# Optimization experiments

Hardware: AMD Instinct MI355X
Metric: run time of the kernel (lower is better)

The kernel has to match this reference:

```python
import jax, jax.numpy as jnp
import numpy as np
from jax import lax

N, EMB, AED, H, KCL = 4096, 768, 512, 8, 32
HD = AED // H
TEMP, THR, EPS, MAX_IT = 0.5, 1e-4, 1e-6, 100


def setup_inputs() -> dict:
    key = jax.random.key(0)
    ks = jax.random.split(key, 9)
    s = 0.02
    return {
        "embeddings": jax.random.normal(ks[0], (N, EMB), jnp.float32),
        "qw": jax.random.normal(ks[1], (EMB, AED), jnp.float32) * s,
        "kw": jax.random.normal(ks[2], (EMB, AED), jnp.float32) * s,
        "vw": jax.random.normal(ks[3], (EMB, AED), jnp.float32) * s,
        "in_proj_w": jax.random.normal(ks[4], (3 * AED, AED), jnp.float32) * s,
        "in_proj_b": jnp.zeros((3 * AED,), jnp.float32),
        "out_w": jax.random.normal(ks[5], (AED, AED), jnp.float32) * s,
        "out_b": jnp.zeros((AED,), jnp.float32),
        "init_idx": jax.random.randint(ks[6], (KCL,), 0, N, dtype=jnp.int32),
    }


def _mha(q, k, v, Wi, bi, Wo, bo):
    # torch nn.MultiheadAttention, batch_first, batch==1, no mask
    Wq, Wk, Wv = jnp.split(Wi, 3, axis=0)
    bq, bk, bv = jnp.split(bi, 3)
    n = q.shape[0]
    qh = (q @ Wq.T + bq).reshape(n, H, HD).transpose(1, 0, 2)  # [H,N,hd]
    kh = (k @ Wk.T + bk).reshape(n, H, HD).transpose(1, 0, 2)
    vh = (v @ Wv.T + bv).reshape(n, H, HD).transpose(1, 0, 2)
    scores = jnp.einsum("hqd,hkd->hqk", qh, kh) / jnp.sqrt(jnp.float32(HD))
    attn = jax.nn.softmax(scores, axis=-1)            # [H,N,N]
    o = jnp.einsum("hqk,hkd->hqd", attn, vh)          # [H,N,hd]
    o = o.transpose(1, 0, 2).reshape(n, AED)
    return o @ Wo.T + bo


def _cdist(X, C):
    # euclidean distance [N,K]
    d2 = (jnp.sum(X * X, 1)[:, None] + jnp.sum(C * C, 1)[None, :]
          - 2.0 * (X @ C.T))
    return jnp.sqrt(jnp.maximum(d2, 0.0))


def _dkm_step(X, C):
    a = jax.nn.softmax(-_cdist(X, C) / TEMP, axis=1)  # [N,K]
    a_sum = jnp.sum(a, axis=0) + EPS                  # [K]
    C_new = (a.T @ X) / a_sum[:, None]                # [K,E]
    return a, C_new


def _dkm(X, C_init):
    a, C_new = _dkm_step(X, C_init)
    diff = jnp.sum(jnp.abs(C_new - C_init))
    def body(carry, _):
        C, a, C_new, diff = carry
        cont = diff > THR
        C2 = jnp.where(cont, C_new, C)
        a2, C_new2 = _dkm_step(X, C2)
        a2 = jnp.where(cont, a2, a)
        C_new2 = jnp.where(cont, C_new2, C_new)
        diff2 = jnp.where(cont, jnp.sum(jnp.abs(C_new2 - C2)), diff)
        return (C2, a2, C_new2, diff2), None
    (C, a, _, _), _ = lax.scan(body, (C_init, a, C_new, diff), None, length=MAX_IT)
    return C, a


def reference(embeddings, qw, kw, vw, in_proj_w, in_proj_b, out_w, out_b, init_idx):
    q = embeddings @ qw
    k = embeddings @ kw
    v = embeddings @ vw
    tr = _mha(q, k, v, in_proj_w, in_proj_b, out_w, out_b)  # [N,AED]
    init_c = lax.stop_gradient(tr[init_idx])                # detached init
    C, a = _dkm(tr, init_c)
    return C, a
```

## Files before the change

### kernel.cpp

```cpp
#include <hip/hip_runtime.h>
#include <hip/hip_bf16.h>


typedef __hip_bfloat16 bf16;
typedef __attribute__((ext_vector_type(8))) short s16x8;
typedef __attribute__((ext_vector_type(4))) float f32x4;

__device__ __forceinline__ void  stv(float* p, float v) { *p = v; }
__device__ __forceinline__ void  stv(bf16*  p, float v) { *p = __float2bfloat16(v); }

__device__ __forceinline__ float gload(const float* p)
{
    return __hip_atomic_load(p, __ATOMIC_RELAXED, __HIP_MEMORY_SCOPE_AGENT);
}
__device__ __forceinline__ void gstore(float* p, float v)
{
    __hip_atomic_store(p, v, __ATOMIC_RELAXED, __HIP_MEMORY_SCOPE_AGENT);
}
__device__ __forceinline__ void gstore2(float2* p, float2 v)
{
    unsigned long long u; __builtin_memcpy(&u, &v, 8);
    __hip_atomic_store((unsigned long long*)p, u, __ATOMIC_RELAXED, __HIP_MEMORY_SCOPE_AGENT);
}

__device__ __forceinline__ unsigned bf16word(float v)
{
    bf16 b = __float2bfloat16(v);
    unsigned short u;
    __builtin_memcpy(&u, &b, 2);
    return ((unsigned)u) << 16;
}

__device__ __forceinline__ void stage8(const float* g, bf16* d)
{
    const float4 a = *(const float4*)g;
    const float4 b = *(const float4*)(g + 4);
    union { uint4 u; bf16 h[8]; } r;
    r.h[0] = __float2bfloat16(a.x); r.h[1] = __float2bfloat16(a.y);
    r.h[2] = __float2bfloat16(a.z); r.h[3] = __float2bfloat16(a.w);
    r.h[4] = __float2bfloat16(b.x); r.h[5] = __float2bfloat16(b.y);
    r.h[6] = __float2bfloat16(b.z); r.h[7] = __float2bfloat16(b.w);
    *(uint4*)d = r.u;
}
__device__ __forceinline__ void stage8(const bf16* g, bf16* d)
{
    *(uint4*)d = *(const uint4*)g;
}
__device__ __forceinline__ void load8f(const float* g, float* v)
{
    const float4 a = *(const float4*)g; const float4 b = *(const float4*)(g + 4);
    v[0]=a.x; v[1]=a.y; v[2]=a.z; v[3]=a.w; v[4]=b.x; v[5]=b.y; v[6]=b.z; v[7]=b.w;
}
__device__ __forceinline__ void load8f(const bf16* g, float* v)
{
    union { uint4 u; bf16 h[8]; } r; r.u = *(const uint4*)g;
#pragma unroll
    for (int j = 0; j < 8; j++) v[j] = __bfloat162float(r.h[j]);
}

struct P3 { const void* a[3]; const void* b[3]; const float* bi[3]; void* c[3]; };

template<typename TA, typename TB, typename TC, bool BT, bool BIAS>
__global__ __launch_bounds__(256) void mgemm(P3 p, int M, int N, int K)
{
    __shared__ __align__(16) bf16 As[64][40];
    __shared__ __align__(16) bf16 Bs[64][40];
    const int z = blockIdx.z;
    const TA* A = (const TA*)p.a[z];
    const TB* B = (const TB*)p.b[z];
    const float* bias = p.bi[z];
    TC* C = (TC*)p.c[z];
    const int m0 = blockIdx.x * 64, n0 = blockIdx.y * 64;
    const int t = threadIdx.x;
    const int w = t >> 6, lane = t & 63, quad = lane >> 4, l15 = lane & 15;
    f32x4 acc[4];
#pragma unroll
    for (int i = 0; i < 4; i++) acc[i] = (f32x4){0.f, 0.f, 0.f, 0.f};
    for (int k0 = 0; k0 < K; k0 += 32) {
        {
            int r = t >> 2, c = (t & 3) * 8;
            stage8(&A[(size_t)(m0 + r) * K + k0 + c], &As[r][c]);
        }
        if constexpr (BT) {
            int r = t >> 2, c = (t & 3) * 8;
            stage8(&B[(size_t)(n0 + r) * K + k0 + c], &Bs[r][c]);
        } else {
            int k = t >> 3, n8 = (t & 7) * 8;
            float v[8];
            load8f(&B[(size_t)(k0 + k) * N + n0 + n8], v);
#pragma unroll
            for (int j = 0; j < 8; j++) Bs[n8 + j][k] = __float2bfloat16(v[j]);
        }
        __syncthreads();
        s16x8 af = *(const s16x8*)&As[w * 16 + l15][quad * 8];
#pragma unroll
        for (int nt = 0; nt < 4; nt++) {
            s16x8 bfv = *(const s16x8*)&Bs[nt * 16 + l15][quad * 8];
            acc[nt] = __builtin_amdgcn_mfma_f32_16x16x32_bf16(af, bfv, acc[nt], 0, 0, 0);
        }
        __syncthreads();
    }
#pragma unroll
    for (int nt = 0; nt < 4; nt++) {
        int col = n0 + nt * 16 + l15;
        float bv = 0.f;
        if constexpr (BIAS) bv = bias[col];
#pragma unroll
        for (int r = 0; r < 4; r++) {
            int row = m0 + w * 16 + quad * 4 + r;
            stv(&C[(size_t)row * N + col], acc[nt][r] + bv);
        }
    }
}

__global__ __launch_bounds__(256) void attn_mfma(
    const bf16* __restrict__ qh, const bf16* __restrict__ kh,
    const bf16* __restrict__ vh, bf16* __restrict__ oatt)
{
    __shared__ __align__(16) bf16  Qs[64][72];
    __shared__ __align__(16) bf16  Ks[64][72];
    __shared__ __align__(16) bf16  Vt[64][72];
    __shared__ __align__(16) float Ss[64][68];
    __shared__ __align__(16) bf16  Ps[64][72];
    __shared__ float mrow[64], lrow[64], arow[64];
    const int bid = blockIdx.x;
    const int h = bid & 7, q0 = (bid >> 3) * 64;
    const int t = threadIdx.x;
    const int w = t >> 6, lane = t & 63, quad = lane >> 4, l15 = lane & 15;

#pragma unroll
    for (int i = 0; i < 2; i++) {
        int idx = t + i * 256;
        int r = idx >> 3, c = (idx & 7) * 8;
        *(uint4*)&Qs[r][c] = *(const uint4*)&qh[(size_t)(q0 + r) * 512 + h * 64 + c];
    }
    if (t < 64) { mrow[t] = -1e30f; lrow[t] = 0.f; }
    f32x4 accO[4];
#pragma unroll
    for (int i = 0; i < 4; i++) accO[i] = (f32x4){0.f, 0.f, 0.f, 0.f};

    const int sidx0 = t, sidx1 = t + 256;
    const int sr0 = sidx0 >> 3, sc0 = (sidx0 & 7) * 8;
    const int sr1 = sidx1 >> 3, sc1v = (sidx1 & 7) * 8;
    uint4 kreg0 = *(const uint4*)&kh[(size_t)sr0 * 512 + h * 64 + sc0];
    uint4 vreg0 = *(const uint4*)&vh[(size_t)sr0 * 512 + h * 64 + sc0];
    uint4 kreg1 = *(const uint4*)&kh[(size_t)sr1 * 512 + h * 64 + sc1v];
    uint4 vreg1 = *(const uint4*)&vh[(size_t)sr1 * 512 + h * 64 + sc1v];

    for (int kb = 0; kb < 4096; kb += 64) {
        __syncthreads();
        {
            *(uint4*)&Ks[sr0][sc0] = kreg0;
            union { uint4 u; bf16 b[8]; } vv; vv.u = vreg0;
            int rlo = sr0 & 7, rch = sr0 >> 3, rx = sidx0 & 7;
#pragma unroll
            for (int j = 0; j < 8; j++)
                Vt[sc0 + j][rlo | (((rch ^ rx) & 7) << 3)] = vv.b[j];
        }
        {
            *(uint4*)&Ks[sr1][sc1v] = kreg1;
            union { uint4 u; bf16 b[8]; } vv; vv.u = vreg1;
            int rlo = sr1 & 7, rch = sr1 >> 3, rx = sidx1 & 7;
#pragma unroll
            for (int j = 0; j < 8; j++)
                Vt[sc1v + j][rlo | (((rch ^ rx) & 7) << 3)] = vv.b[j];
        }
        __syncthreads();
        if (kb + 64 < 4096) {
            size_t base0 = (size_t)(kb + 64 + sr0) * 512 + h * 64;
            size_t base1 = (size_t)(kb + 64 + sr1) * 512 + h * 64;
            kreg0 = *(const uint4*)&kh[base0 + sc0];
            vreg0 = *(const uint4*)&vh[base0 + sc0];
            kreg1 = *(const uint4*)&kh[base1 + sc1v];
            vreg1 = *(const uint4*)&vh[base1 + sc1v];
        }
        f32x4 accS[4];
#pragma unroll
        for (int i = 0; i < 4; i++) accS[i] = (f32x4){0.f, 0.f, 0.f, 0.f};
        __builtin_amdgcn_s_setprio(1);
#pragma unroll
        for (int dc = 0; dc < 64; dc += 32) {
            s16x8 aq = *(const s16x8*)&Qs[w * 16 + l15][dc + quad * 8];
#pragma unroll
            for (int nt = 0; nt < 4; nt++) {
                s16x8 bk = *(const s16x8*)&Ks[nt * 16 + l15][dc + quad * 8];
                accS[nt] = __builtin_amdgcn_mfma_f32_16x16x32_bf16(aq, bk, accS[nt], 0, 0, 0);
            }
        }
        __builtin_amdgcn_s_setprio(0);
#pragma unroll
        for (int nt = 0; nt < 4; nt++)
#pragma unroll
            for (int r = 0; r < 4; r++)
                Ss[w * 16 + quad * 4 + r][nt * 16 + l15] = accS[nt][r] * 0.1803368801f;
        {
            const int srow = t >> 2, sseg = t & 3;
            float* sp = &Ss[srow][sseg * 16];
            float4 s0 = *(const float4*)(sp + 0);
            float4 s1 = *(const float4*)(sp + 4);
            float4 s2 = *(const float4*)(sp + 8);
            float4 s3 = *(const float4*)(sp + 12);
            float mold = mrow[srow];
            float m01 = fmaxf(fmaxf(s0.x, s0.y), fmaxf(s0.z, s0.w));
            float m23 = fmaxf(fmaxf(s1.x, s1.y), fmaxf(s1.z, s1.w));
            float m45 = fmaxf(fmaxf(s2.x, s2.y), fmaxf(s2.z, s2.w));
            float m67 = fmaxf(fmaxf(s3.x, s3.y), fmaxf(s3.z, s3.w));
            float mx = fmaxf(fmaxf(m01, m23), fmaxf(m45, m67));
            mx = fmaxf(mx, mold);
            mx = fmaxf(mx, __shfl_xor(mx, 1));
            mx = fmaxf(mx, __shfl_xor(mx, 2));
            s0.x = exp2f(s0.x - mx); s0.y = exp2f(s0.y - mx);
            s0.z = exp2f(s0.z - mx); s0.w = exp2f(s0.w - mx);
            s1.x = exp2f(s1.x - mx); s1.y = exp2f(s1.y - mx);
            s1.z = exp2f(s1.z - mx); s1.w = exp2f(s1.w - mx);
            s2.x = exp2f(s2.x - mx); s2.y = exp2f(s2.y - mx);
            s2.z = exp2f(s2.z - mx); s2.w = exp2f(s2.w - mx);
            s3.x = exp2f(s3.x - mx); s3.y = exp2f(s3.y - mx);
            s3.z = exp2f(s3.z - mx); s3.w = exp2f(s3.w - mx);
            union { uint4 u; bf16 h[8]; } pa, pb;
            pa.h[0] = __float2bfloat16(s0.x); pa.h[1] = __float2bfloat16(s0.y);
            pa.h[2] = __float2bfloat16(s0.z); pa.h[3] = __float2bfloat16(s0.w);
            pa.h[4] = __float2bfloat16(s1.x); pa.h[5] = __float2bfloat16(s1.y);
            pa.h[6] = __float2bfloat16(s1.z); pa.h[7] = __float2bfloat16(s1.w);
            pb.h[0] = __float2bfloat16(s2.x); pb.h[1] = __float2bfloat16(s2.y);
            pb.h[2] = __float2bfloat16(s2.z); pb.h[3] = __float2bfloat16(s2.w);
            pb.h[4] = __float2bfloat16(s3.x); pb.h[5] = __float2bfloat16(s3.y);
            pb.h[6] = __float2bfloat16(s3.z); pb.h[7] = __float2bfloat16(s3.w);
            *(uint4*)&Ps[srow][sseg * 16]     = pa.u;
            *(uint4*)&Ps[srow][sseg * 16 + 8] = pb.u;
            float ps = (s0.x + s0.y + s0.z + s0.w) + (s1.x + s1.y + s1.z + s1.w)
                     + (s2.x + s2.y + s2.z + s2.w) + (s3.x + s3.y + s3.z + s3.w);
            ps += __shfl_xor(ps, 1);
            ps += __shfl_xor(ps, 2);
            if (sseg == 0) {
                float al = exp2f(mold - mx);
                lrow[srow] = lrow[srow] * al + ps;
                mrow[srow] = mx;
                arow[srow] = al;
            }
        }
        float al4[4];
#pragma unroll
        for (int r = 0; r < 4; r++) al4[r] = arow[w * 16 + quad * 4 + r];
#pragma unroll
        for (int dt = 0; dt < 4; dt++)
#pragma unroll
            for (int r = 0; r < 4; r++) accO[dt][r] *= al4[r];
        __builtin_amdgcn_s_setprio(1);
#pragma unroll
        for (int kc = 0; kc < 64; kc += 32) {
            s16x8 pf = *(const s16x8*)&Ps[w * 16 + l15][kc + quad * 8];
#pragma unroll
            for (int dt = 0; dt < 4; dt++) {
                int vrow = dt * 16 + l15;
                s16x8 bv = *(const s16x8*)&Vt[vrow][((((kc >> 3) + quad) ^ (vrow >> 3)) & 7) << 3];
                accO[dt] = __builtin_amdgcn_mfma_f32_16x16x32_bf16(pf, bv, accO[dt], 0, 0, 0);
            }
        }
        __builtin_amdgcn_s_setprio(0);
    }
#pragma unroll
    for (int dt = 0; dt < 4; dt++)
#pragma unroll
        for (int r = 0; r < 4; r++) {
            int row = w * 16 + quad * 4 + r;
            oatt[(size_t)(q0 + row) * 512 + h * 64 + dt * 16 + l15] =
                __float2bfloat16(accO[dt][r] / lrow[row]);
        }
}

__global__ __launch_bounds__(64) void k_bar_init(unsigned* bar, unsigned* gen)
{
    if (threadIdx.x < 9) bar[threadIdx.x] = 0u;
    if (threadIdx.x == 0) *gen = 0u;
}

__device__ __forceinline__ void gridbar(unsigned* bar, unsigned* gen)
{
    __syncthreads();
    if (threadIdx.x == 0) {
        unsigned g = __hip_atomic_load(gen, __ATOMIC_RELAXED, __HIP_MEMORY_SCOPE_AGENT);
        const int sub = blockIdx.x & 7;
        bool released = false;
        if (__hip_atomic_fetch_add(&bar[sub], 1u, __ATOMIC_RELAXED, __HIP_MEMORY_SCOPE_AGENT) == 15u) {
            __hip_atomic_store(&bar[sub], 0u, __ATOMIC_RELAXED, __HIP_MEMORY_SCOPE_AGENT);
            asm volatile("s_waitcnt vmcnt(0)" ::: "memory");
            if (__hip_atomic_fetch_add(&bar[8], 1u, __ATOMIC_RELAXED, __HIP_MEMORY_SCOPE_AGENT) == 7u) {
                __hip_atomic_store(&bar[8], 0u, __ATOMIC_RELAXED, __HIP_MEMORY_SCOPE_AGENT);
                asm volatile("s_waitcnt vmcnt(0)" ::: "memory");
                __hip_atomic_fetch_add(gen, 1u, __ATOMIC_RELAXED, __HIP_MEMORY_SCOPE_AGENT);
                released = true;
            }
        }
        if (!released) {
            while (__hip_atomic_load(gen, __ATOMIC_RELAXED, __HIP_MEMORY_SCOPE_AGENT) == g)
                __builtin_amdgcn_s_sleep(1);
        }
    }
    __syncthreads();
}

__global__ __launch_bounds__(256) void dkm_persist(
    const float* __restrict__ X, const int* __restrict__ idxp,
    float* __restrict__ Cacc, float* __restrict__ Cb0, float* __restrict__ Cb1,
    float* __restrict__ asumb, float* __restrict__ diffb, float* __restrict__ cnormb,
    unsigned* bar, unsigned* gen, unsigned* __restrict__ out)
{
    const int b = blockIdx.x, t = threadIdx.x;
    const int n0 = b * 32;
    __shared__ float Cs[128][32];
    __shared__ float as_[32][32];
    __shared__ float red[256];
    __shared__ float xn[32];

    {
        int rl = t >> 3, j = t & 7;
        const float* p = X + (size_t)(n0 + rl) * 512 + j * 64;
        float s = 0.f;
#pragma unroll
        for (int i = 0; i < 64; i++) { float v = p[i]; s += v * v; }
        as_[rl][j] = s;
        __syncthreads();
        if (t < 32) {
            float tot = 0.f;
#pragma unroll
            for (int jj = 0; jj < 8; jj++) tot += as_[t][jj];
            xn[t] = tot;
        }
        if (t < 128) {
            int o = b * 128 + t;
            gstore(&Cb0[o], X[(size_t)idxp[o & 31] * 512 + (o >> 5)]);
        }
        int z = b * 256 + t;
        if (z < 3072) gstore(&asumb[z], 0.f);
        if (z < 97)   gstore(&diffb[z], 0.f);
        if (z < 3136) gstore(&cnormb[z], 0.f);
    }
    gridbar(bar, gen);
    if (b < 32) {
        float s = 0.f;
        for (int e = t; e < 512; e += 256) { float v = gload(&Cb0[e * 32 + b]); s += v * v; }
        red[t] = s; __syncthreads();
        for (int st = 128; st > 0; st >>= 1) { if (t < st) red[t] += red[t + st]; __syncthreads(); }
        if (t == 0) gstore(&cnormb[b], red[0]);
    }
    gridbar(bar, gen);

    const int k = t & 31, rg = t >> 5;
    int ifin = 96;
    float pre[16];
#pragma unroll
    for (int j = 0; j < 16; j++) pre[j] = gload(&Cb0[t + j * 256]);
    for (int i = 0; i <= 96; i++) {
        const float* Cc = (i & 1) ? Cb1 : Cb0;
        float* Cn = (i & 1) ? Cb0 : Cb1;
        float dots[4] = {0.f, 0.f, 0.f, 0.f};
        for (int ec = 0; ec < 4; ec++) {
            __syncthreads();
#pragma unroll
            for (int j = 0; j < 16; j++) {
                int idx = t + j * 256;
                Cs[idx >> 5][idx & 31] = pre[j];
            }
            __syncthreads();
            if (ec < 3) {
#pragma unroll
                for (int j = 0; j < 16; j++)
                    pre[j] = gload(&Cc[(ec + 1) * 4096 + t + j * 256]);
            }
            const float* xb = X + (size_t)(n0 + rg) * 512 + ec * 128;
#pragma unroll 4
            for (int ee4 = 0; ee4 < 128; ee4 += 4) {
                float4 x0 = *(const float4*)&xb[ee4];
                float4 x1 = *(const float4*)&xb[8 * 512 + ee4];
                float4 x2 = *(const float4*)&xb[16 * 512 + ee4];
                float4 x3 = *(const float4*)&xb[24 * 512 + ee4];
                {
                    float cv = Cs[ee4 + 0][k];
                    dots[0] += x0.x * cv; dots[1] += x1.x * cv;
                    dots[2] += x2.x * cv; dots[3] += x3.x * cv;
                }
                {
                    float cv = Cs[ee4 + 1][k];
                    dots[0] += x0.y * cv; dots[1] += x1.y * cv;
                    dots[2] += x2.y * cv; dots[3] += x3.y * cv;
                }
                {
                    float cv = Cs[ee4 + 2][k];
                    dots[0] += x0.z * cv; dots[1] += x1.z * cv;
                    dots[2] += x2.z * cv; dots[3] += x3.z * cv;
                }
                {
                    float cv = Cs[ee4 + 3][k];
                    dots[0] += x0.w * cv; dots[1] += x1.w * cv;
                    dots[2] += x2.w * cv; dots[3] += x3.w * cv;
                }
            }
        }
        float cn = gload(&cnormb[i * 32 + k]);
#pragma unroll
        for (int rr = 0; rr < 4; rr++) {
            int rl = rg + rr * 8;
            float d2 = xn[rl] + cn - 2.f * dots[rr];
            as_[rl][k] = -2.f * sqrtf(fmaxf(d2, 0.f));
        }
        __syncthreads();
        if (t < 32) {
            float mx = -1e30f;
            for (int kk = 0; kk < 32; kk++) mx = fmaxf(mx, as_[t][kk]);
            float su = 0.f;
            for (int kk = 0; kk < 32; kk++) su += expf(as_[t][kk] - mx);
            float inv = 1.f / su;
            for (int kk = 0; kk < 32; kk++) as_[t][kk] = expf(as_[t][kk] - mx) * inv;
        }
        __syncthreads();
        if (i == 96) {
#pragma unroll
            for (int i2 = 0; i2 < 4; i2++) {
                int o = t + i2 * 256;
                int r = o >> 5, kk = o & 31;
                out[16384 + (n0 + r) * 32 + kk] = bf16word(as_[r][kk]);
            }
            break;
        }
        if (t < 32) {
            float s = 0.f;
            for (int r = 0; r < 32; r++) s += as_[r][t];
            atomicAdd(&asumb[i * 32 + t], s);
        }
        {
            float acc[64];
#pragma unroll
            for (int i2 = 0; i2 < 64; i2++) acc[i2] = 0.f;
            const float2* X2 = (const float2*)(X + (size_t)n0 * 512);
            for (int r = 0; r < 32; r++) {
                float2 xv = X2[r * 256 + t];
                const float4* ar4 = (const float4*)as_[r];
#pragma unroll
                for (int kq = 0; kq < 8; kq++) {
                    float4 av = ar4[kq];
                    acc[(kq * 4 + 0) * 2 + 0] += av.x * xv.x; acc[(kq * 4 + 0) * 2 + 1] += av.x * xv.y;
                    acc[(kq * 4 + 1) * 2 + 0] += av.y * xv.x; acc[(kq * 4 + 1) * 2 + 1] += av.y * xv.y;
                    acc[(kq * 4 + 2) * 2 + 0] += av.z * xv.x; acc[(kq * 4 + 2) * 2 + 1] += av.z * xv.y;
                    acc[(kq * 4 + 3) * 2 + 0] += av.w * xv.x; acc[(kq * 4 + 3) * 2 + 1] += av.w * xv.y;
                }
            }
            float2* cb = (float2*)(Cacc + (size_t)b * 16384);
#pragma unroll
            for (int k2 = 0; k2 < 32; k2++) {
                float2 wv; wv.x = acc[k2 * 2 + 0]; wv.y = acc[k2 * 2 + 1];
                gstore2(&cb[k2 * 256 + t], wv);
            }
        }
        gridbar(bar, gen);
        {
            const int j = t & 127, half = t >> 7;
            const int o = b * 128 + j;
            float s = 0.f;
            for (int p = half * 64; p < half * 64 + 64; p++) s += gload(&Cacc[(size_t)p * 16384 + o]);
            red[t] = s;
            __syncthreads();
            float df = 0.f, cp = 0.f;
            if (t < 128) {
                float tot = red[t] + red[t + 128];
                int kk = o >> 9, e = o & 511;
                float cn2 = tot / (gload(&asumb[i * 32 + kk]) + 1e-6f);
                gstore(&Cn[e * 32 + kk], cn2);
                df = fabsf(cn2 - gload(&Cc[e * 32 + kk]));
                cp = cn2 * cn2;
            }
            __syncthreads();
            red[t] = df; __syncthreads();
            for (int st = 128; st > 0; st >>= 1) { if (t < st) red[t] += red[t + st]; __syncthreads(); }
            if (t == 0) atomicAdd(&diffb[i], red[0]);
            __syncthreads();
            red[t] = cp; __syncthreads();
            for (int st = 128; st > 0; st >>= 1) { if (t < st) red[t] += red[t + st]; __syncthreads(); }
            if (t == 0) atomicAdd(&cnormb[(i + 1) * 32 + (b >> 2)], red[0]);
        }
        gridbar(bar, gen);
        if (!(gload(&diffb[i]) > 1e-4f)) {
            ifin = i;
#pragma unroll
            for (int i2 = 0; i2 < 4; i2++) {
                int o = t + i2 * 256;
                int r = o >> 5, kk = o & 31;
                out[16384 + (n0 + r) * 32 + kk] = bf16word(as_[r][kk]);
            }
            break;
        }
#pragma unroll
        for (int j = 0; j < 16; j++) pre[j] = gload(&Cn[t + j * 256]);
    }
    {
        const float* Cf = (ifin & 1) ? Cb1 : Cb0;
        if (t < 128) {
            int idx = b * 128 + t;
            int kk = idx >> 9, e = idx & 511;
            out[idx] = bf16word(gload(&Cf[e * 32 + kk]));
        }
    }
}

extern "C" void kernel_launch(void* const* d_in, const int* in_sizes, int n_in,
                              void* d_out, int out_size, void* d_ws, size_t ws_size,
                              hipStream_t stream)
{
    const size_t NEED = 25323292;
    if (ws_size < NEED) return;

    const float* emb = (const float*)d_in[0];
    const float* qw  = (const float*)d_in[1];
    const float* kw  = (const float*)d_in[2];
    const float* vw  = (const float*)d_in[3];
    const float* ipw = (const float*)d_in[4];
    const float* ipb = (const float*)d_in[5];
    const float* ow  = (const float*)d_in[6];
    const float* ob  = (const float*)d_in[7];
    const int*   idx = (const int*)d_in[8];
    unsigned* out = (unsigned*)d_out;

    float* ws    = (float*)d_ws;
    bf16*  qkv   = (bf16*)ws;
    bf16*  weff  = (bf16*)(ws + 3145728);
    bf16*  oatt  = (bf16*)(ws + 3145728);
    float* X     = ws;
    float* Cacc  = ws + 4194304;
    float* Cb0   = ws + 6291456;
    float* Cb1   = ws + 6307840;
    float* asumb = ws + 6324224;
    float* diffb = ws + 6327456;
    float* cnormb= ws + 6327557;
    unsigned* bar = (unsigned*)(ws + 6324224 + 3072);
    unsigned* gen = (unsigned*)(ws + 6330822);

    bf16* qh = qkv;
    bf16* kh = qkv + 2097152;
    bf16* vh = qkv + 4194304;

    k_bar_init<<<1, 64, 0, stream>>>(bar, gen);

    P3 pw;
    pw.a[0] = qw;  pw.a[1] = kw;  pw.a[2] = vw;
    pw.b[0] = ipw; pw.b[1] = ipw + 262144; pw.b[2] = ipw + 524288;
    pw.bi[0] = pw.bi[1] = pw.bi[2] = nullptr;
    pw.c[0] = weff; pw.c[1] = weff + 393216; pw.c[2] = weff + 786432;
    mgemm<float, float, bf16, true, false><<<dim3(12, 8, 3), 256, 0, stream>>>(pw, 768, 512, 512);

    P3 pq;
    pq.a[0] = pq.a[1] = pq.a[2] = emb;
    pq.b[0] = weff; pq.b[1] = weff + 393216; pq.b[2] = weff + 786432;
    pq.bi[0] = ipb; pq.bi[1] = ipb + 512; pq.bi[2] = ipb + 1024;
    pq.c[0] = qh; pq.c[1] = kh; pq.c[2] = vh;
    mgemm<float, bf16, bf16, false, true><<<dim3(64, 8, 3), 256, 0, stream>>>(pq, 4096, 512, 768);

    attn_mfma<<<dim3(512), 256, 0, stream>>>(qh, kh, vh, oatt);

    P3 pt;
    pt.a[0] = oatt; pt.b[0] = ow; pt.bi[0] = ob; pt.c[0] = X;
    pt.a[1] = pt.a[2] = pt.b[1] = pt.b[2] = nullptr;
    pt.bi[1] = pt.bi[2] = nullptr; pt.c[1] = pt.c[2] = nullptr;
    mgemm<bf16, float, float, true, true><<<dim3(64, 8, 1), 256, 0, stream>>>(pt, 4096, 512, 512);

    dkm_persist<<<dim3(128), 256, 0, stream>>>(X, idx, Cacc, Cb0, Cb1,
                                               asumb, diffb, cnormb, bar, gen, out);
}
```

Measured before the change: 448.1 us.

## Double-buffer K/V tiles in attention and broadcast convergence flag through grid barrier

```diff
diff --git a/kernel.cpp b/kernel.cpp
--- a/kernel.cpp
+++ b/kernel.cpp
@@ -118,8 +118,8 @@
     const bf16* __restrict__ vh, bf16* __restrict__ oatt)
 {
     __shared__ __align__(16) bf16  Qs[64][72];
-    __shared__ __align__(16) bf16  Ks[64][72];
-    __shared__ __align__(16) bf16  Vt[64][72];
+    __shared__ __align__(16) bf16  Ks[2][64][72];
+    __shared__ __align__(16) bf16  Vt[2][64][72];
     __shared__ __align__(16) float Ss[64][68];
     __shared__ __align__(16) bf16  Ps[64][72];
     __shared__ float mrow[64], lrow[64], arow[64];
@@ -146,33 +146,60 @@
     uint4 vreg0 = *(const uint4*)&vh[(size_t)sr0 * 512 + h * 64 + sc0];
     uint4 kreg1 = *(const uint4*)&kh[(size_t)sr1 * 512 + h * 64 + sc1v];
     uint4 vreg1 = *(const uint4*)&vh[(size_t)sr1 * 512 + h * 64 + sc1v];
-
-    for (int kb = 0; kb < 4096; kb += 64) {
-        __syncthreads();
-        {
-            *(uint4*)&Ks[sr0][sc0] = kreg0;
-            union { uint4 u; bf16 b[8]; } vv; vv.u = vreg0;
-            int rlo = sr0 & 7, rch = sr0 >> 3, rx = sidx0 & 7;
-#pragma unroll
-            for (int j = 0; j < 8; j++)
-                Vt[sc0 + j][rlo | (((rch ^ rx) & 7) << 3)] = vv.b[j];
-        }
-        {
-            *(uint4*)&Ks[sr1][sc1v] = kreg1;
-            union { uint4 u; bf16 b[8]; } vv; vv.u = vreg1;
-            int rlo = sr1 & 7, rch = sr1 >> 3, rx = sidx1 & 7;
-#pragma unroll
-            for (int j = 0; j < 8; j++)
-                Vt[sc1v + j][rlo | (((rch ^ rx) & 7) << 3)] = vv.b[j];
-        }
-        __syncthreads();
-        if (kb + 64 < 4096) {
-            size_t base0 = (size_t)(kb + 64 + sr0) * 512 + h * 64;
-            size_t base1 = (size_t)(kb + 64 + sr1) * 512 + h * 64;
-            kreg0 = *(const uint4*)&kh[base0 + sc0];
-            vreg0 = *(const uint4*)&vh[base0 + sc0];
-            kreg1 = *(const uint4*)&kh[base1 + sc1v];
-            vreg1 = *(const uint4*)&vh[base1 + sc1v];
+    {
+        *(uint4*)&Ks[0][sr0][sc0] = kreg0;
+        union { uint4 u; bf16 b[8]; } vv; vv.u = vreg0;
+        int rlo = sr0 & 7, rch = sr0 >> 3, rx = sidx0 & 7;
+#pragma unroll
+        for (int j = 0; j < 8; j++)
+            Vt[0][sc0 + j][rlo | (((rch ^ rx) & 7) << 3)] = vv.b[j];
+    }
+    {
+        *(uint4*)&Ks[0][sr1][sc1v] = kreg1;
+        union { uint4 u; bf16 b[8]; } vv; vv.u = vreg1;
+        int rlo = sr1 & 7, rch = sr1 >> 3, rx = sidx1 & 7;
+#pragma unroll
+        for (int j = 0; j < 8; j++)
+            Vt[0][sc1v + j][rlo | (((rch ^ rx) & 7) << 3)] = vv.b[j];
+    }
+    {
+        size_t base0 = (size_t)(64 + sr0) * 512 + h * 64;
+        size_t base1 = (size_t)(64 + sr1) * 512 + h * 64;
+        kreg0 = *(const uint4*)&kh[base0 + sc0];
+        vreg0 = *(const uint4*)&vh[base0 + sc0];
+        kreg1 = *(const uint4*)&kh[base1 + sc1v];
+        vreg1 = *(const uint4*)&vh[base1 + sc1v];
+    }
+    __syncthreads();
+
+    for (int s = 0; s < 64; s++) {
+        const int cur = s & 1;
+        if (s + 1 < 64) {
+            const int nxt = cur ^ 1;
+            {
+                *(uint4*)&Ks[nxt][sr0][sc0] = kreg0;
+                union { uint4 u; bf16 b[8]; } vv; vv.u = vreg0;
+                int rlo = sr0 & 7, rch = sr0 >> 3, rx = sidx0 & 7;
+#pragma unroll
+                for (int j = 0; j < 8; j++)
+                    Vt[nxt][sc0 + j][rlo | (((rch ^ rx) & 7) << 3)] = vv.b[j];
+            }
+            {
+                *(uint4*)&Ks[nxt][sr1][sc1v] = kreg1;
+                union { uint4 u; bf16 b[8]; } vv; vv.u = vreg1;
+                int rlo = sr1 & 7, rch = sr1 >> 3, rx = sidx1 & 7;
+#pragma unroll
+                for (int j = 0; j < 8; j++)
+                    Vt[nxt][sc1v + j][rlo | (((rch ^ rx) & 7) << 3)] = vv.b[j];
+            }
+            if (s + 2 < 64) {
+                size_t base0 = (size_t)((s + 2) * 64 + sr0) * 512 + h * 64;
+                size_t base1 = (size_t)((s + 2) * 64 + sr1) * 512 + h * 64;
+                kreg0 = *(const uint4*)&kh[base0 + sc0];
+                vreg0 = *(const uint4*)&vh[base0 + sc0];
+                kreg1 = *(const uint4*)&kh[base1 + sc1v];
+                vreg1 = *(const uint4*)&vh[base1 + sc1v];
+            }
         }
         f32x4 accS[4];
 #pragma unroll
@@ -183,7 +210,7 @@
             s16x8 aq = *(const s16x8*)&Qs[w * 16 + l15][dc + quad * 8];
 #pragma unroll
             for (int nt = 0; nt < 4; nt++) {
-                s16x8 bk = *(const s16x8*)&Ks[nt * 16 + l15][dc + quad * 8];
+                s16x8 bk = *(const s16x8*)&Ks[cur][nt * 16 + l15][dc + quad * 8];
                 accS[nt] = __builtin_amdgcn_mfma_f32_16x16x32_bf16(aq, bk, accS[nt], 0, 0, 0);
             }
         }
@@ -253,11 +280,12 @@
 #pragma unroll
             for (int dt = 0; dt < 4; dt++) {
                 int vrow = dt * 16 + l15;
-                s16x8 bv = *(const s16x8*)&Vt[vrow][((((kc >> 3) + quad) ^ (vrow >> 3)) & 7) << 3];
+                s16x8 bv = *(const s16x8*)&Vt[cur][vrow][((((kc >> 3) + quad) ^ (vrow >> 3)) & 7) << 3];
                 accO[dt] = __builtin_amdgcn_mfma_f32_16x16x32_bf16(pf, bv, accO[dt], 0, 0, 0);
             }
         }
         __builtin_amdgcn_s_setprio(0);
+        __syncthreads();
     }
 #pragma unroll
     for (int dt = 0; dt < 4; dt++)
@@ -275,29 +303,42 @@
     if (threadIdx.x == 0) *gen = 0u;
 }
 
-__device__ __forceinline__ void gridbar(unsigned* bar, unsigned* gen)
+__device__ __forceinline__ unsigned gridbar_f(unsigned* bar, unsigned* gen,
+                                              const float* dptr, float thr,
+                                              unsigned* bcast)
 {
     __syncthreads();
     if (threadIdx.x == 0) {
         unsigned g = __hip_atomic_load(gen, __ATOMIC_RELAXED, __HIP_MEMORY_SCOPE_AGENT);
         const int sub = blockIdx.x & 7;
+        unsigned newg = 0;
         bool released = false;
         if (__hip_atomic_fetch_add(&bar[sub], 1u, __ATOMIC_RELAXED, __HIP_MEMORY_SCOPE_AGENT) == 15u) {
             __hip_atomic_store(&bar[sub], 0u, __ATOMIC_RELAXED, __HIP_MEMORY_SCOPE_AGENT);
             asm volatile("s_waitcnt vmcnt(0)" ::: "memory");
             if (__hip_atomic_fetch_add(&bar[8], 1u, __ATOMIC_RELAXED, __HIP_MEMORY_SCOPE_AGENT) == 7u) {
                 __hip_atomic_store(&bar[8], 0u, __ATOMIC_RELAXED, __HIP_MEMORY_SCOPE_AGENT);
+                unsigned flag = 0u;
+                if (dptr) flag = (gload(dptr) > thr) ? 1u : 0u;
                 asm volatile("s_waitcnt vmcnt(0)" ::: "memory");
-                __hip_atomic_fetch_add(gen, 1u, __ATOMIC_RELAXED, __HIP_MEMORY_SCOPE_AGENT);
+                newg = (((g >> 1) + 1u) << 1) | flag;
+                __hip_atomic_store(gen, newg, __ATOMIC_RELAXED, __HIP_MEMORY_SCOPE_AGENT);
                 released = true;
             }
         }
         if (!released) {
-            while (__hip_atomic_load(gen, __ATOMIC_RELAXED, __HIP_MEMORY_SCOPE_AGENT) == g)
+            unsigned ng;
+            do {
+                ng = __hip_atomic_load(gen, __ATOMIC_RELAXED, __HIP_MEMORY_SCOPE_AGENT);
+                if ((ng >> 1) != (g >> 1)) break;
                 __builtin_amdgcn_s_sleep(1);
-        }
+            } while (true);
+            newg = ng;
+        }
+        *bcast = newg;
     }
     __syncthreads();
+    return *bcast & 1u;
 }
 
 __global__ __launch_bounds__(256) void dkm_persist(
@@ -312,6 +353,7 @@
     __shared__ float as_[32][32];
     __shared__ float red[256];
     __shared__ float xn[32];
+    __shared__ unsigned gw;
 
     {
         int rl = t >> 3, j = t & 7;
@@ -336,7 +378,7 @@
         if (z < 97)   gstore(&diffb[z], 0.f);
         if (z < 3136) gstore(&cnormb[z], 0.f);
     }
-    gridbar(bar, gen);
+    gridbar_f(bar, gen, nullptr, 0.f, &gw);
     if (b < 32) {
         float s = 0.f;
         for (int e = t; e < 512; e += 256) { float v = gload(&Cb0[e * 32 + b]); s += v * v; }
@@ -344,7 +386,7 @@
         for (int st = 128; st > 0; st >>= 1) { if (t < st) red[t] += red[t + st]; __syncthreads(); }
         if (t == 0) gstore(&cnormb[b], red[0]);
     }
-    gridbar(bar, gen);
+    gridbar_f(bar, gen, nullptr, 0.f, &gw);
 
     const int k = t & 31, rg = t >> 5;
     int ifin = 96;
@@ -452,7 +494,7 @@
                 gstore2(&cb[k2 * 256 + t], wv);
             }
         }
-        gridbar(bar, gen);
+        gridbar_f(bar, gen, nullptr, 0.f, &gw);
         {
             const int j = t & 127, half = t >> 7;
             const int o = b * 128 + j;
@@ -478,8 +520,8 @@
             for (int st = 128; st > 0; st >>= 1) { if (t < st) red[t] += red[t + st]; __syncthreads(); }
             if (t == 0) atomicAdd(&cnormb[(i + 1) * 32 + (b >> 2)], red[0]);
         }
-        gridbar(bar, gen);
-        if (!(gload(&diffb[i]) > 1e-4f)) {
+        unsigned cont = gridbar_f(bar, gen, &diffb[i], 1e-4f, &gw);
+        if (!cont) {
             ifin = i;
 #pragma unroll
             for (int i2 = 0; i2 < 4; i2++) {
```

Result: no change. 450.8 us (+0.6%).
